# Kernel tuning notes

Measured on AMD Instinct MI355X. Metric: run time of the kernel, lower is better.

The kernel has to match this reference:

```python
import jax, jax.numpy as jnp
import numpy as np
from jax import lax

B, P, ENC = 64, 196, 2048
E, H, A, V = 512, 512, 512, 10000
L = 21  # caption length -> T = 20 decode steps


def setup_inputs() -> dict:
    key = jax.random.key(0)
    ks = jax.random.split(key, 20)
    s = 0.02
    inp = {
        "features": jax.random.normal(ks[0], (B, P, ENC), jnp.float32),
        "captions": jax.random.randint(ks[1], (B, L), 0, V),
        # attention
        "W_enc_att": jax.random.normal(ks[2], (ENC, A), jnp.float32) * s,
        "b_enc_att": jnp.zeros((A,), jnp.float32),
        "W_dec_att": jax.random.normal(ks[3], (H, A), jnp.float32) * s,
        "b_dec_att": jnp.zeros((A,), jnp.float32),
        "W_full": jax.random.normal(ks[4], (A, 1), jnp.float32) * s,
        "b_full": jnp.zeros((1,), jnp.float32),
        # embedding (uniform(-0.1, 0.1) as in init_weights)
        "emb": jax.random.uniform(ks[5], (V, E), jnp.float32, -0.1, 0.1),
        # LSTMCell: input = embed + encoder_dim, gate order i,f,g,o
        "W_ih": jax.random.normal(ks[6], (E + ENC, 4 * H), jnp.float32) * s,
        "W_hh": jax.random.normal(ks[7], (H, 4 * H), jnp.float32) * s,
        "b_ih": jnp.zeros((4 * H,), jnp.float32),
        "b_hh": jnp.zeros((4 * H,), jnp.float32),
        # init state projections
        "W_init_h": jax.random.normal(ks[8], (ENC, H), jnp.float32) * s,
        "b_init_h": jnp.zeros((H,), jnp.float32),
        "W_init_c": jax.random.normal(ks[9], (ENC, H), jnp.float32) * s,
        "b_init_c": jnp.zeros((H,), jnp.float32),
        # gating
        "W_fbeta": jax.random.normal(ks[10], (H, ENC), jnp.float32) * s,
        "b_fbeta": jnp.zeros((ENC,), jnp.float32),
        # output fc (uniform(-0.1,0.1), bias 0)
        "W_fc": jax.random.uniform(ks[11], (H, V), jnp.float32, -0.1, 0.1),
        "b_fc": jnp.zeros((V,), jnp.float32),
    }
    return inp


def reference(features, captions, W_enc_att, b_enc_att, W_dec_att, b_dec_att,
              W_full, b_full, emb, W_ih, W_hh, b_ih, b_hh,
              W_init_h, b_init_h, W_init_c, b_init_c,
              W_fbeta, b_fbeta, W_fc, b_fc):
    # init hidden state from mean-pooled encoder features
    mean_enc = features.mean(axis=1)                       # [B, ENC]
    h0 = mean_enc @ W_init_h + b_init_h                    # [B, H]
    c0 = mean_enc @ W_init_c + b_init_c

    # encoder-side attention projection is time-invariant: precompute
    att1 = features @ W_enc_att + b_enc_att                # [B, P, A]

    T = captions.shape[1] - 1                              # decode_lengths = L-1 (equal lengths)
    embs = emb[captions[:, :T]]                            # [B, T, E]
    embs_t = jnp.swapaxes(embs, 0, 1)                      # [T, B, E]

    def step(carry, e_t):
        h, c = carry
        att2 = h @ W_dec_att + b_dec_att                   # [B, A]
        scores = (jax.nn.relu(att1 + att2[:, None, :]) @ W_full)[..., 0] + b_full  # [B, P]
        alpha = jax.nn.softmax(scores, axis=1)
        awe = jnp.einsum('bp,bpe->be', alpha, features)    # [B, ENC]
        gate = jax.nn.sigmoid(h @ W_fbeta + b_fbeta)
        awe = gate * awe
        x = jnp.concatenate([e_t, awe], axis=1)            # [B, E+ENC]
        gates = x @ W_ih + h @ W_hh + b_ih + b_hh          # [B, 4H]
        i, f, g, o = jnp.split(gates, 4, axis=1)
        c_new = jax.nn.sigmoid(f) * c + jax.nn.sigmoid(i) * jnp.tanh(g)
        h_new = jax.nn.sigmoid(o) * jnp.tanh(c_new)
        preds = h_new @ W_fc + b_fc                        # dropout in eval mode = identity
        return (h_new, c_new), preds

    _, preds = lax.scan(step, (h0, c0), embs_t)            # [T, B, V]
    return jnp.swapaxes(preds, 0, 1)                       # [B, T, V]
```

## Files before the change

### kernel.cpp

```cpp
#include <hip/hip_runtime.h>
#include <hip/hip_bf16.h>


#define TB 256

typedef __bf16 bf16x8 __attribute__((ext_vector_type(8)));
typedef float f32x4 __attribute__((ext_vector_type(4)));
typedef unsigned short u16x8 __attribute__((ext_vector_type(8)));
typedef unsigned short u16x4 __attribute__((ext_vector_type(4)));
typedef unsigned short ushort_t;

__device__ __forceinline__ ushort_t f2bf(float x) {
    unsigned u = __builtin_bit_cast(unsigned, x);
    u += 0x7fffu + ((u >> 16) & 1u);
    return (ushort_t)(u >> 16);
}
__device__ __forceinline__ float bf2f(ushort_t b) {
    return __builtin_bit_cast(float, (unsigned)b << 16);
}
__device__ __forceinline__ void store_pack(
    ushort_t* __restrict__ Ph, ushort_t* __restrict__ Pl,
    int KC, int m, int k, float v)
{
    const size_t flat = ((((size_t)(m >> 4) * KC + (k >> 5)) * 64)
                         + ((k & 31) >> 3) * 16 + (m & 15)) * 8 + (k & 7);
    const ushort_t h = f2bf(v);
    Ph[flat] = h;
    Pl[flat] = f2bf(v - bf2f(h));
}

struct PackJobs {
    const float* W[7];
    ushort_t* Bh[7];
    ushort_t* Bl[7];
    int Nsrc[7], ntCount[7], KC[7], ntBase[7];
    int cum[8];
};

__global__ __launch_bounds__(TB) void pack_all(PackJobs J)
{
    const int blk = blockIdx.x;
    int j = 0;
    #pragma unroll
    for (int i = 1; i < 7; ++i) if (blk >= J.cum[i]) j = i;
    const int g = (blk - J.cum[j]) * TB + threadIdx.x;
    const int KC = J.KC[j];
    const int lane = g & 63;
    const int kc = (g >> 6) % KC;
    const int nt = g / (64 * KC);
    if (nt >= J.ntCount[j]) return;
    const int Nsrc = J.Nsrc[j];
    const float* W = J.W[j];
    const int n = nt * 16 + (lane & 15);
    const int kb = kc * 32 + (lane >> 4) * 8;
    u16x8 hv, lv;
    #pragma unroll
    for (int e = 0; e < 8; ++e) {
        const float x = (n < Nsrc) ? W[(size_t)(kb + e) * Nsrc + n] : 0.f;
        const ushort_t h = f2bf(x);
        hv[e] = h;
        lv[e] = f2bf(x - bf2f(h));
    }
    const size_t flat = (((size_t)(J.ntBase[j] + nt) * KC + kc) * 64 + lane) * 8;
    *(u16x8*)&J.Bh[j][flat] = hv;
    *(u16x8*)&J.Bl[j][flat] = lv;
}

__global__ __launch_bounds__(TB) void feat2bf(
    const float* __restrict__ f, ushort_t* __restrict__ fbf)
{
    const size_t i8 = ((size_t)blockIdx.x * TB + threadIdx.x) * 8;
    const float4 a = *(const float4*)&f[i8];
    const float4 b = *(const float4*)&f[i8 + 4];
    u16x8 v;
    v[0] = f2bf(a.x); v[1] = f2bf(a.y); v[2] = f2bf(a.z); v[3] = f2bf(a.w);
    v[4] = f2bf(b.x); v[5] = f2bf(b.y); v[6] = f2bf(b.z); v[7] = f2bf(b.w);
    *(u16x8*)&fbf[i8] = v;
}

template<int MT, int NT, int WR, int WC>
__device__ __forceinline__ void mfma_tile(
    const ushort_t* lds, int wr, int wc, int lane,
    f32x4 acc[MT / WR][NT / WC])
{
    constexpr int MFR = MT / WR, NFR = NT / WC;
    bf16x8 ah[MFR], al[MFR];
    #pragma unroll
    for (int i = 0; i < MFR; ++i) {
        ah[i] = __builtin_bit_cast(bf16x8, *(const u16x8*)&lds[(wr * MFR + i) * 512 + lane * 8]);
        al[i] = __builtin_bit_cast(bf16x8, *(const u16x8*)&lds[(MT + wr * MFR + i) * 512 + lane * 8]);
    }
    #pragma unroll
    for (int j = 0; j < NFR; ++j) {
        const bf16x8 bh = __builtin_bit_cast(bf16x8, *(const u16x8*)&lds[(2 * MT + wc * NFR + j) * 512 + lane * 8]);
        const bf16x8 bl = __builtin_bit_cast(bf16x8, *(const u16x8*)&lds[(2 * MT + NT + wc * NFR + j) * 512 + lane * 8]);
        #pragma unroll
        for (int i = 0; i < MFR; ++i) {
            acc[i][j] = __builtin_amdgcn_mfma_f32_16x16x32_bf16(ah[i], bh, acc[i][j], 0, 0, 0);
            acc[i][j] = __builtin_amdgcn_mfma_f32_16x16x32_bf16(ah[i], bl, acc[i][j], 0, 0, 0);
            acc[i][j] = __builtin_amdgcn_mfma_f32_16x16x32_bf16(al[i], bh, acc[i][j], 0, 0, 0);
        }
    }
}

template<int MT, int NT, int WR, int WC>
__global__ __launch_bounds__(TB) void gemm_mfma(
    const ushort_t* __restrict__ Ah, const ushort_t* __restrict__ Al,
    const ushort_t* __restrict__ Bh, const ushort_t* __restrict__ Bl,
    int KC, int kcPer,
    const float* __restrict__ bias,
    float* __restrict__ C, int ldc, int Ncols, size_t cPartStride)
{
    constexpr int MFR = MT / WR, NFR = NT / WC, CH = 2 * (MT + NT);
    __shared__ __align__(16) ushort_t lds[CH * 512];
    const int tid = threadIdx.x, wid = tid >> 6, lane = tid & 63;
    const int wr = wid / WC, wc = wid % WC;

    const int tot = gridDim.x * gridDim.y;
    const int lin = blockIdx.x + gridDim.x * blockIdx.y;
    const int q = tot >> 3, r = tot & 7;
    const int xcd = lin & 7, jj = lin >> 3;
    const int base = (xcd < r) ? xcd * (q + 1) : r * (q + 1) + (xcd - r) * q;
    const int lin2 = base + jj;
    const int nb = lin2 / gridDim.y;
    const int mb = lin2 % gridDim.y;

    const int kc0 = blockIdx.z * kcPer;

    f32x4 acc[MFR][NFR];
    #pragma unroll
    for (int i = 0; i < MFR; ++i)
        #pragma unroll
        for (int j = 0; j < NFR; ++j)
            acc[i][j] = f32x4{0.f, 0.f, 0.f, 0.f};

    for (int kc = kc0; kc < kc0 + kcPer; ++kc) {
        __syncthreads();
        #pragma unroll
        for (int cc = 0; cc < CH / 4; ++cc) {
            const int c = cc * 4 + wid;
            const ushort_t* src;
            if (c < MT)                src = Ah + ((size_t)(mb * MT + c) * KC + kc) * 512;
            else if (c < 2 * MT)       src = Al + ((size_t)(mb * MT + c - MT) * KC + kc) * 512;
            else if (c < 2 * MT + NT)  src = Bh + ((size_t)(nb * NT + c - 2 * MT) * KC + kc) * 512;
            else                       src = Bl + ((size_t)(nb * NT + c - 2 * MT - NT) * KC + kc) * 512;
            *(u16x8*)&lds[c * 512 + lane * 8] = *(const u16x8*)(src + lane * 8);
        }
        __syncthreads();
        mfma_tile<MT, NT, WR, WC>(lds, wr, wc, lane, acc);
    }

    C += (size_t)blockIdx.z * cPartStride;
    #pragma unroll
    for (int i = 0; i < MFR; ++i)
        #pragma unroll
        for (int j = 0; j < NFR; ++j) {
            const int col = nb * NT * 16 + (wc * NFR + j) * 16 + (lane & 15);
            if (col < Ncols) {
                const float bv = bias ? bias[col] : 0.f;
                const int rbase = mb * MT * 16 + (wr * MFR + i) * 16 + ((lane >> 4) << 2);
                #pragma unroll
                for (int r2 = 0; r2 < 4; ++r2)
                    C[(size_t)(rbase + r2) * ldc + col] = acc[i][j][r2] + bv;
            }
        }
}

__global__ __launch_bounds__(TB) void gemm_att1(
    const ushort_t* __restrict__ fbf,
    const ushort_t* __restrict__ Bh, const ushort_t* __restrict__ Bl,
    const float* __restrict__ bias, ushort_t* __restrict__ att1bf)
{
    __shared__ __align__(16) ushort_t lds[20 * 512];
    const int tid = threadIdx.x, wid = tid >> 6, lane = tid & 63;
    const int wr = wid >> 1, wc = wid & 1;

    const int lin = blockIdx.x + (blockIdx.y << 2);
    const int lin2 = (lin & 7) * 98 + (lin >> 3);
    const int nb = lin2 & 3, mb = lin2 >> 2;

    f32x4 acc[2][4];
    #pragma unroll
    for (int i = 0; i < 2; ++i)
        #pragma unroll
        for (int j = 0; j < 4; ++j)
            acc[i][j] = f32x4{0.f, 0.f, 0.f, 0.f};

    const int arow = tid >> 2, akg = tid & 3;
    const size_t abase = (size_t)(mb * 64 + arow) * 2048 + akg * 8;
    const int aldst = (arow >> 4) * 512 + (akg * 16 + (arow & 15)) * 8;

    for (int kc = 0; kc < 64; ++kc) {
        __syncthreads();
        #pragma unroll
        for (int cc = 0; cc < 4; ++cc) {
            const int c = cc * 4 + wid;
            const ushort_t* src = (c < 8)
                ? Bh + ((size_t)(nb * 8 + c) * 64 + kc) * 512
                : Bl + ((size_t)(nb * 8 + c - 8) * 64 + kc) * 512;
            *(u16x8*)&lds[(4 + c) * 512 + lane * 8] = *(const u16x8*)(src + lane * 8);
        }
        *(u16x8*)&lds[aldst] = *(const u16x8*)&fbf[abase + (size_t)kc * 32];
        __syncthreads();

        bf16x8 ah[2];
        #pragma unroll
        for (int i = 0; i < 2; ++i)
            ah[i] = __builtin_bit_cast(bf16x8, *(const u16x8*)&lds[(wr * 2 + i) * 512 + lane * 8]);
        #pragma unroll
        for (int j = 0; j < 4; ++j) {
            const bf16x8 bh = __builtin_bit_cast(bf16x8, *(const u16x8*)&lds[(4 + wc * 4 + j) * 512 + lane * 8]);
            const bf16x8 bl = __builtin_bit_cast(bf16x8, *(const u16x8*)&lds[(12 + wc * 4 + j) * 512 + lane * 8]);
            #pragma unroll
            for (int i = 0; i < 2; ++i) {
                acc[i][j] = __builtin_amdgcn_mfma_f32_16x16x32_bf16(ah[i], bh, acc[i][j], 0, 0, 0);
                acc[i][j] = __builtin_amdgcn_mfma_f32_16x16x32_bf16(ah[i], bl, acc[i][j], 0, 0, 0);
            }
        }
    }

    #pragma unroll
    for (int i = 0; i < 2; ++i)
        #pragma unroll
        for (int j = 0; j < 4; ++j) {
            const int col = nb * 128 + (wc * 4 + j) * 16 + (lane & 15);
            const float bv = bias[col];
            const int rbase = mb * 64 + (wr * 2 + i) * 16 + ((lane >> 4) << 2);
            #pragma unroll
            for (int r = 0; r < 4; ++r)
                att1bf[(size_t)(rbase + r) * 512 + col] = f2bf(acc[i][j][r] + bv);
        }
}

__device__ __forceinline__ void gemm_body(
    float (*As)[68], float (*Ws)[68],
    const float* __restrict__ A, int lda,
    const float* __restrict__ W, int ldw,
    float* __restrict__ C, int ldc,
    int nTile, int N, int K)
{
    const int tid = threadIdx.x;
    const int tn = tid & 15;
    const int tm = tid >> 4;
    const int n0 = nTile * 64;

    float acc[4][4] = {{0.f}};

    for (int k0 = 0; k0 < K; k0 += 32) {
        {
            int r  = tid >> 3;
            int cc = (tid & 7) * 4;
            #pragma unroll
            for (int rr = 0; rr < 64; rr += 32) {
                const float4 a = *(const float4*)&A[(size_t)(rr + r) * lda + (k0 + cc)];
                As[cc + 0][rr + r] = a.x;
                As[cc + 1][rr + r] = a.y;
                As[cc + 2][rr + r] = a.z;
                As[cc + 3][rr + r] = a.w;
            }
        }
        {
            int r  = tid >> 4;
            int cc = (tid & 15) * 4;
            #pragma unroll
            for (int rr = 0; rr < 32; rr += 16) {
                const float4 w = *(const float4*)&W[(size_t)(k0 + rr + r) * ldw + (n0 + cc)];
                *(float4*)&Ws[rr + r][cc] = w;
            }
        }
        __syncthreads();
        #pragma unroll
        for (int kk = 0; kk < 32; ++kk) {
            const float4 a = *(const float4*)&As[kk][tm * 4];
            const float4 w = *(const float4*)&Ws[kk][tn * 4];
            const float av[4] = {a.x, a.y, a.z, a.w};
            const float wv[4] = {w.x, w.y, w.z, w.w};
            #pragma unroll
            for (int i = 0; i < 4; ++i)
                #pragma unroll
                for (int j = 0; j < 4; ++j)
                    acc[i][j] = fmaf(av[i], wv[j], acc[i][j]);
        }
        __syncthreads();
    }

    #pragma unroll
    for (int i = 0; i < 4; ++i) {
        const int m = tm * 4 + i;
        #pragma unroll
        for (int j = 0; j < 4; ++j)
            C[(size_t)m * ldc + (n0 + tn * 4 + j)] = acc[i][j];
    }
}

__global__ __launch_bounds__(TB) void gemm_hc(
    const float* __restrict__ mean,
    const float* __restrict__ Wh0, const float* __restrict__ Wc0,
    float* __restrict__ h0p, float* __restrict__ c0p)
{
    __shared__ float As[32][68];
    __shared__ float Ws[32][68];
    const int ks = blockIdx.y & 7;
    const int which = blockIdx.y >> 3;
    const float* W = which ? Wc0 : Wh0;
    float* Cp = which ? c0p : h0p;
    gemm_body(As, Ws,
              mean + (size_t)ks * 256, 2048,
              W + (size_t)ks * 256 * 512, 512,
              Cp + (size_t)ks * 64 * 512, 512,
              blockIdx.x, 512, 256);
}

__global__ __launch_bounds__(TB) void scores_k(
    const ushort_t* __restrict__ att1bf,
    const float* __restrict__ hga_part,
    const float* __restrict__ bd,
    const float* __restrict__ Wfull,
    float* __restrict__ scores)
{
    const int b = blockIdx.x;
    const int tid = threadIdx.x;
    const int wave = tid >> 6;
    const int lane = tid & 63;

    __shared__ float a2[512];
    __shared__ float wf[512];

    for (int i = tid; i < 512; i += TB) {
        float v = bd[i];
        #pragma unroll
        for (int s = 0; s < 4; ++s)
            v += hga_part[(size_t)s * 64 * 4608 + (size_t)b * 4608 + i];
        a2[i] = v;
        wf[i] = Wfull[i];
    }
    __syncthreads();

    const int k0 = lane * 8;
    float a2r[8], wfr[8];
    #pragma unroll
    for (int e = 0; e < 8; ++e) { a2r[e] = a2[k0 + e]; wfr[e] = wf[k0 + e]; }

    const int p0 = blockIdx.y * 28 + wave * 7;
    #pragma unroll
    for (int pp = 0; pp < 7; ++pp) {
        const int p = p0 + pp;
        const u16x8 v = *(const u16x8*)&att1bf[((size_t)b * 196 + p) * 512 + k0];
        float s = 0.f;
        #pragma unroll
        for (int e = 0; e < 8; ++e)
            s = fmaf(fmaxf(bf2f(v[e]) + a2r[e], 0.f), wfr[e], s);
        #pragma unroll
        for (int o = 32; o; o >>= 1) s += __shfl_xor(s, o);
        if (lane == 0) scores[b * 196 + p] = s;
    }
}

__global__ __launch_bounds__(512) void awe_gate(
    const float* __restrict__ scores,
    const ushort_t* __restrict__ fbf,
    const float* __restrict__ hga_part,
    const float* __restrict__ bf,
    ushort_t* __restrict__ gPh, ushort_t* __restrict__ gPl)
{
    const int b = blockIdx.y, chunk = blockIdx.x;
    const int tid = threadIdx.x;
    const int q = tid >> 6, lane = tid & 63;

    __shared__ float al[196];
    __shared__ float redm[8], reds[8];
    __shared__ float smq[8][512];

    const float sv = (tid < 196) ? scores[b * 196 + tid] : -1e30f;
    float m = sv;
    #pragma unroll
    for (int o = 32; o; o >>= 1) m = fmaxf(m, __shfl_xor(m, o));
    if (lane == 0) redm[q] = m;
    __syncthreads();
    m = redm[0];
    #pragma unroll
    for (int i = 1; i < 8; ++i) m = fmaxf(m, redm[i]);

    const float e = (tid < 196) ? expf(sv - m) : 0.f;
    float s = e;
    #pragma unroll
    for (int o = 32; o; o >>= 1) s += __shfl_xor(s, o);
    if (lane == 0) reds[q] = s;
    __syncthreads();
    s = reds[0];
    #pragma unroll
    for (int i = 1; i < 8; ++i) s += reds[i];

    if (tid < 196) al[tid] = e / s;
    __syncthreads();

    const int col0 = chunk * 512 + lane * 8;
    const ushort_t* f = fbf + (size_t)b * 196 * 2048 + col0;
    float acc[8] = {0.f, 0.f, 0.f, 0.f, 0.f, 0.f, 0.f, 0.f};
    const int p0 = q * 25;
    const int pn = (q == 7) ? 21 : 25;
    for (int pp = 0; pp < pn; ++pp) {
        const float w = al[p0 + pp];
        const u16x8 v = *(const u16x8*)&f[(size_t)(p0 + pp) * 2048];
        #pragma unroll
        for (int ee = 0; ee < 8; ++ee)
            acc[ee] = fmaf(w, bf2f(v[ee]), acc[ee]);
    }
    *(f32x4*)&smq[q][lane * 8]     = f32x4{acc[0], acc[1], acc[2], acc[3]};
    *(f32x4*)&smq[q][lane * 8 + 4] = f32x4{acc[4], acc[5], acc[6], acc[7]};
    __syncthreads();

    const int eg = chunk * 512 + tid;
    float a = smq[0][tid];
    #pragma unroll
    for (int i = 1; i < 8; ++i) a += smq[i][tid];
    float gp = bf[eg];
    #pragma unroll
    for (int ss = 0; ss < 4; ++ss)
        gp += hga_part[(size_t)ss * 64 * 4608 + (size_t)b * 4608 + 512 + eg];
    const float gate = 1.f / (1.f + expf(-gp));
    store_pack(gPh, gPl, 64, b, eg, gate * a);
}

__global__ __launch_bounds__(TB) void lstm_pw(
    const float* __restrict__ gates_part,
    const float* __restrict__ hga_part,
    const float* __restrict__ eW,
    const float* __restrict__ b_hh,
    int t,
    float* __restrict__ c,
    ushort_t* __restrict__ hPh, ushort_t* __restrict__ hPl,
    ushort_t* __restrict__ sPh, ushort_t* __restrict__ sPl)
{
    const int idx = blockIdx.x * TB + threadIdx.x;
    const int b = idx >> 9;
    const int j = idx & 511;

    float g[4];
    #pragma unroll
    for (int comp = 0; comp < 4; ++comp) {
        const int col = comp * 512 + j;
        float v = b_hh[col] + eW[((size_t)b * 20 + t) * 2048 + col];
        #pragma unroll
        for (int s = 0; s < 8; ++s)
            v += gates_part[(size_t)s * 64 * 2048 + (size_t)b * 2048 + col];
        #pragma unroll
        for (int s = 0; s < 4; ++s)
            v += hga_part[(size_t)s * 64 * 4608 + (size_t)b * 4608 + 2560 + col];
        g[comp] = v;
    }
    const float si = 1.f / (1.f + expf(-g[0]));
    const float sf = 1.f / (1.f + expf(-g[1]));
    const float gg = tanhf(g[2]);
    const float so = 1.f / (1.f + expf(-g[3]));
    const float cn = sf * c[idx] + si * gg;
    c[idx] = cn;
    const float hn = so * tanhf(cn);
    store_pack(hPh, hPl, 16, b, j, hn);
    store_pack(sPh, sPl, 16, b * 20 + t, j, hn);
}

__global__ __launch_bounds__(TB) void mean_feat(
    const float* __restrict__ features, float* __restrict__ mean_enc)
{
    const int b = blockIdx.y;
    const int e = blockIdx.x * TB + threadIdx.x;
    const float* f = features + (size_t)b * 196 * 2048 + e;
    float s = 0.f;
    #pragma unroll 4
    for (int p = 0; p < 196; ++p) s += f[(size_t)p * 2048];
    mean_enc[b * 2048 + e] = s * (1.f / 196.f);
}

__global__ __launch_bounds__(TB) void gather_emb_pack(
    const int* __restrict__ captions,
    const float* __restrict__ emb,
    ushort_t* __restrict__ Ph, ushort_t* __restrict__ Pl)
{
    const int bt = blockIdx.x;
    const int b = bt / 20;
    const int t = bt % 20;
    const int tok = captions[b * 21 + t];
    for (int e = threadIdx.x; e < 512; e += TB)
        store_pack(Ph, Pl, 16, bt, e, emb[(size_t)tok * 512 + e]);
}

__global__ __launch_bounds__(TB) void reduce_hc(
    const float* __restrict__ h0p, const float* __restrict__ c0p,
    const float* __restrict__ bh0, const float* __restrict__ bc0,
    ushort_t* __restrict__ hPh, ushort_t* __restrict__ hPl,
    float* __restrict__ c)
{
    const int idx = blockIdx.x * TB + threadIdx.x;
    const int half = idx >> 15;
    const int i = idx & 32767;
    const int j = i & 511;
    const float* P = half ? c0p : h0p;
    float v = half ? bc0[j] : bh0[j];
    #pragma unroll
    for (int s = 0; s < 8; ++s) v += P[(size_t)s * 64 * 512 + i];
    if (half) c[i] = v;
    else      store_pack(hPh, hPl, 16, i >> 9, j, v);
}

extern "C" void kernel_launch(void* const* d_in, const int* in_sizes, int n_in,
                              void* d_out, int out_size, void* d_ws, size_t ws_size,
                              hipStream_t stream)
{
    const float* features  = (const float*)d_in[0];
    const int*   captions  = (const int*)  d_in[1];
    const float* W_enc_att = (const float*)d_in[2];
    const float* b_enc_att = (const float*)d_in[3];
    const float* W_dec_att = (const float*)d_in[4];
    const float* b_dec_att = (const float*)d_in[5];
    const float* W_full    = (const float*)d_in[6];
    const float* emb       = (const float*)d_in[8];
    const float* W_ih      = (const float*)d_in[9];
    const float* W_hh      = (const float*)d_in[10];
    const float* b_ih      = (const float*)d_in[11];
    const float* b_hh      = (const float*)d_in[12];
    const float* W_init_h  = (const float*)d_in[13];
    const float* b_init_h  = (const float*)d_in[14];
    const float* W_init_c  = (const float*)d_in[15];
    const float* b_init_c  = (const float*)d_in[16];
    const float* W_fbeta   = (const float*)d_in[17];
    const float* b_fbeta   = (const float*)d_in[18];
    const float* W_fc      = (const float*)d_in[19];
    const float* b_fc      = (const float*)d_in[20];
    float* out = (float*)d_out;
    (void)ws_size;

    float* ws = (float*)d_ws;
    size_t off = 0;
    auto alloc  = [&](size_t n) { float* p = ws + off; off += n; return p; };
    auto ualloc = [&](size_t n) { ushort_t* p = (ushort_t*)(ws + off); off += (n + 1) / 2; return p; };

    float* eW     = alloc((size_t)64 * 20 * 2048);
    float* mean   = alloc(64 * 2048);
    float* hga    = alloc((size_t)4 * 64 * 4608);
    float* gatesp = alloc((size_t)8 * 64 * 2048);
    float* c      = alloc(64 * 512);
    float* scores = alloc(64 * 196);

    ushort_t* fbf    = ualloc((size_t)12544 * 2048);
    ushort_t* att1bf = ualloc((size_t)12544 * 512);
    ushort_t* WencH = ualloc((size_t)32 * 64 * 512);
    ushort_t* WencL = ualloc((size_t)32 * 64 * 512);
    ushort_t* WtopH = ualloc((size_t)128 * 16 * 512);
    ushort_t* WtopL = ualloc((size_t)128 * 16 * 512);
    ushort_t* Wih2H = ualloc((size_t)128 * 64 * 512);
    ushort_t* Wih2L = ualloc((size_t)128 * 64 * 512);
    ushort_t* WdfhH = ualloc((size_t)288 * 16 * 512);
    ushort_t* WdfhL = ualloc((size_t)288 * 16 * 512);
    ushort_t* WfcH  = ualloc((size_t)632 * 16 * 512);
    ushort_t* WfcL  = ualloc((size_t)632 * 16 * 512);
    ushort_t* embsH = ualloc((size_t)80 * 16 * 512);
    ushort_t* embsL = ualloc((size_t)80 * 16 * 512);
    ushort_t* hPh   = ualloc((size_t)4 * 16 * 512);
    ushort_t* hPl   = ualloc((size_t)4 * 16 * 512);
    ushort_t* gPh   = ualloc((size_t)4 * 64 * 512);
    ushort_t* gPl   = ualloc((size_t)4 * 64 * 512);
    ushort_t* sPh   = ualloc((size_t)80 * 16 * 512);
    ushort_t* sPl   = ualloc((size_t)80 * 16 * 512);

    float* h0p = hga;
    float* c0p = gatesp;

    PackJobs J;
    J.W[0]=W_enc_att;               J.Bh[0]=WencH; J.Bl[0]=WencL; J.Nsrc[0]=512;   J.ntCount[0]=32;  J.KC[0]=64; J.ntBase[0]=0;
    J.W[1]=W_ih;                    J.Bh[1]=WtopH; J.Bl[1]=WtopL; J.Nsrc[1]=2048;  J.ntCount[1]=128; J.KC[1]=16; J.ntBase[1]=0;
    J.W[2]=W_ih + (size_t)512*2048; J.Bh[2]=Wih2H; J.Bl[2]=Wih2L; J.Nsrc[2]=2048;  J.ntCount[2]=128; J.KC[2]=64; J.ntBase[2]=0;
    J.W[3]=W_dec_att;               J.Bh[3]=WdfhH; J.Bl[3]=WdfhL; J.Nsrc[3]=512;   J.ntCount[3]=32;  J.KC[3]=16; J.ntBase[3]=0;
    J.W[4]=W_fbeta;                 J.Bh[4]=WdfhH; J.Bl[4]=WdfhL; J.Nsrc[4]=2048;  J.ntCount[4]=128; J.KC[4]=16; J.ntBase[4]=32;
    J.W[5]=W_hh;                    J.Bh[5]=WdfhH; J.Bl[5]=WdfhL; J.Nsrc[5]=2048;  J.ntCount[5]=128; J.KC[5]=16; J.ntBase[5]=160;
    J.W[6]=W_fc;                    J.Bh[6]=WfcH;  J.Bl[6]=WfcL;  J.Nsrc[6]=10000; J.ntCount[6]=632; J.KC[6]=16; J.ntBase[6]=0;
    {
        int cum = 0;
        const int blks[7] = {512, 512, 2048, 128, 512, 512, 2528};
        for (int i = 0; i < 7; ++i) { J.cum[i] = cum; cum += blks[i]; }
        J.cum[7] = cum;
        pack_all<<<cum, TB, 0, stream>>>(J);
    }

    feat2bf<<<12544, TB, 0, stream>>>(features, fbf);
    gather_emb_pack<<<1280, TB, 0, stream>>>(captions, emb, embsH, embsL);
    mean_feat<<<dim3(8, 64), TB, 0, stream>>>(features, mean);
    gemm_hc<<<dim3(8, 16), TB, 0, stream>>>(mean, W_init_h, W_init_c, h0p, c0p);
    reduce_hc<<<256, TB, 0, stream>>>(h0p, c0p, b_init_h, b_init_c, hPh, hPl, c);
    gemm_att1<<<dim3(4, 196), TB, 0, stream>>>(fbf, WencH, WencL, b_enc_att, att1bf);
    gemm_mfma<8, 8, 2, 2><<<dim3(16, 10, 1), TB, 0, stream>>>(
        embsH, embsL, WtopH, WtopL, 16, 16, b_ih, eW, 2048, 2048, 0);

    for (int t = 0; t < 20; ++t) {
        gemm_mfma<4, 8, 2, 2><<<dim3(36, 1, 4), TB, 0, stream>>>(
            hPh, hPl, WdfhH, WdfhL, 16, 4, nullptr, hga, 4608, 4608, (size_t)64 * 4608);
        scores_k<<<dim3(64, 7), TB, 0, stream>>>(att1bf, hga, b_dec_att, W_full, scores);
        awe_gate<<<dim3(4, 64), 512, 0, stream>>>(scores, fbf, hga, b_fbeta, gPh, gPl);
        gemm_mfma<4, 8, 2, 2><<<dim3(16, 1, 8), TB, 0, stream>>>(
            gPh, gPl, Wih2H, Wih2L, 64, 8, nullptr, gatesp, 2048, 2048, (size_t)64 * 2048);
        lstm_pw<<<128, TB, 0, stream>>>(gatesp, hga, eW, b_hh, t, c, hPh, hPl, sPh, sPl);
    }

    gemm_mfma<8, 8, 2, 2><<<dim3(79, 10, 1), TB, 0, stream>>>(
        sPh, sPl, WfcH, WfcL, 16, 16, b_fc, out, 10000, 10000, 0);
}
```

Before: 1.056 ms.

## Double-buffer att1 GEMM LDS with register prefetch; compute mean from bf16 features

gemm_att1 now processes two K-chunks per iteration into a double-buffered LDS region. It prefetches the next tiles into registers while the MFMAs run on the current buffer, which halves the barriers and hides global load latency. mean_feat now reads the bf16 copy of the features instead of fp32, halving the bytes it reads. The bf16 mean adds rounding error to the initial h/c, and the larger LDS footprint may reduce occupancy.

Measured after the change: 1.051 ms. About the same (-0.4%).

```diff
diff --git a/kernel.cpp b/kernel.cpp
--- a/kernel.cpp
+++ b/kernel.cpp
@@ -171,7 +171,7 @@
     const ushort_t* __restrict__ Bh, const ushort_t* __restrict__ Bl,
     const float* __restrict__ bias, ushort_t* __restrict__ att1bf)
 {
-    __shared__ __align__(16) ushort_t lds[20 * 512];
+    __shared__ __align__(16) ushort_t lds[2 * 40 * 512];
     const int tid = threadIdx.x, wid = tid >> 6, lane = tid & 63;
     const int wr = wid >> 1, wc = wid & 1;
 
@@ -188,35 +188,65 @@
 
     const int arow = tid >> 2, akg = tid & 3;
     const size_t abase = (size_t)(mb * 64 + arow) * 2048 + akg * 8;
-    const int aldst = (arow >> 4) * 512 + (akg * 16 + (arow & 15)) * 8;
-
-    for (int kc = 0; kc < 64; ++kc) {
+    const int aldst = (akg * 16 + (arow & 15)) * 8;
+    const int achunk = arow >> 4;
+
+    u16x8 regs[10];
+
+    auto issue = [&](int kc2) {
+        #pragma unroll
+        for (int cc = 0; cc < 8; ++cc) {
+            const int s = cc * 4 + wid;
+            const int kcoff = s & 1, ch = s >> 1;
+            const ushort_t* src = (ch < 8)
+                ? Bh + ((size_t)(nb * 8 + ch) * 64 + kc2 + kcoff) * 512
+                : Bl + ((size_t)(nb * 8 + (ch - 8)) * 64 + kc2 + kcoff) * 512;
+            regs[cc] = *(const u16x8*)(src + lane * 8);
+        }
+        regs[8] = *(const u16x8*)&fbf[abase + (size_t)kc2 * 32];
+        regs[9] = *(const u16x8*)&fbf[abase + (size_t)(kc2 + 1) * 32];
+    };
+    auto commit = [&](ushort_t* buf) {
+        #pragma unroll
+        for (int cc = 0; cc < 8; ++cc) {
+            const int s = cc * 4 + wid;
+            *(u16x8*)&buf[(8 + s) * 512 + lane * 8] = regs[cc];
+        }
+        *(u16x8*)&buf[achunk * 512 + aldst] = regs[8];
+        *(u16x8*)&buf[(4 + achunk) * 512 + aldst] = regs[9];
+    };
+
+    issue(0);
+    commit(lds);
+    __syncthreads();
+
+    int cur = 0;
+    for (int kc2 = 0; kc2 < 64; kc2 += 2) {
+        const bool more = (kc2 + 2 < 64);
+        if (more) issue(kc2 + 2);
+
+        const ushort_t* buf = lds + cur * 40 * 512;
+        #pragma unroll
+        for (int kcoff = 0; kcoff < 2; ++kcoff) {
+            bf16x8 ah[2];
+            #pragma unroll
+            for (int i = 0; i < 2; ++i)
+                ah[i] = __builtin_bit_cast(bf16x8, *(const u16x8*)&buf[(kcoff * 4 + wr * 2 + i) * 512 + lane * 8]);
+            #pragma unroll
+            for (int j = 0; j < 4; ++j) {
+                const bf16x8 bh = __builtin_bit_cast(bf16x8, *(const u16x8*)&buf[(8 + (wc * 4 + j) * 2 + kcoff) * 512 + lane * 8]);
+                const bf16x8 bl = __builtin_bit_cast(bf16x8, *(const u16x8*)&buf[(8 + (8 + wc * 4 + j) * 2 + kcoff) * 512 + lane * 8]);
+                #pragma unroll
+                for (int i = 0; i < 2; ++i) {
+                    acc[i][j] = __builtin_amdgcn_mfma_f32_16x16x32_bf16(ah[i], bh, acc[i][j], 0, 0, 0);
+                    acc[i][j] = __builtin_amdgcn_mfma_f32_16x16x32_bf16(ah[i], bl, acc[i][j], 0, 0, 0);
+                }
+            }
+        }
+
+        if (more) commit(lds + (cur ^ 1) * 40 * 512);
         __syncthreads();
-        #pragma unroll
-        for (int cc = 0; cc < 4; ++cc) {
-            const int c = cc * 4 + wid;
-            const ushort_t* src = (c < 8)
-                ? Bh + ((size_t)(nb * 8 + c) * 64 + kc) * 512
-                : Bl + ((size_t)(nb * 8 + c - 8) * 64 + kc) * 512;
-            *(u16x8*)&lds[(4 + c) * 512 + lane * 8] = *(const u16x8*)(src + lane * 8);
-        }
-        *(u16x8*)&lds[aldst] = *(const u16x8*)&fbf[abase + (size_t)kc * 32];
-        __syncthreads();
-
-        bf16x8 ah[2];
-        #pragma unroll
-        for (int i = 0; i < 2; ++i)
-            ah[i] = __builtin_bit_cast(bf16x8, *(const u16x8*)&lds[(wr * 2 + i) * 512 + lane * 8]);
-        #pragma unroll
-        for (int j = 0; j < 4; ++j) {
-            const bf16x8 bh = __builtin_bit_cast(bf16x8, *(const u16x8*)&lds[(4 + wc * 4 + j) * 512 + lane * 8]);
-            const bf16x8 bl = __builtin_bit_cast(bf16x8, *(const u16x8*)&lds[(12 + wc * 4 + j) * 512 + lane * 8]);
-            #pragma unroll
-            for (int i = 0; i < 2; ++i) {
-                acc[i][j] = __builtin_amdgcn_mfma_f32_16x16x32_bf16(ah[i], bh, acc[i][j], 0, 0, 0);
-                acc[i][j] = __builtin_amdgcn_mfma_f32_16x16x32_bf16(ah[i], bl, acc[i][j], 0, 0, 0);
-            }
-        }
+        cur ^= 1;
     }
 
     #pragma unroll
@@ -460,15 +490,15 @@
     store_pack(sPh, sPl, 16, b * 20 + t, j, hn);
 }
 
-__global__ __launch_bounds__(TB) void mean_feat(
-    const float* __restrict__ features, float* __restrict__ mean_enc)
+__global__ __launch_bounds__(TB) void mean_feat_bf(
+    const ushort_t* __restrict__ fbf, float* __restrict__ mean_enc)
 {
     const int b = blockIdx.y;
     const int e = blockIdx.x * TB + threadIdx.x;
-    const float* f = features + (size_t)b * 196 * 2048 + e;
+    const ushort_t* f = fbf + (size_t)b * 196 * 2048 + e;
     float s = 0.f;
     #pragma unroll 4
-    for (int p = 0; p < 196; ++p) s += f[(size_t)p * 2048];
+    for (int p = 0; p < 196; ++p) s += bf2f(f[(size_t)p * 2048]);
     mean_enc[b * 2048 + e] = s * (1.f / 196.f);
 }
 
@@ -584,7 +614,7 @@
 
     feat2bf<<<12544, TB, 0, stream>>>(features, fbf);
     gather_emb_pack<<<1280, TB, 0, stream>>>(captions, emb, embsH, embsL);
-    mean_feat<<<dim3(8, 64), TB, 0, stream>>>(features, mean);
+    mean_feat_bf<<<dim3(8, 64), TB, 0, stream>>>(fbf, mean);
     gemm_hc<<<dim3(8, 16), TB, 0, stream>>>(mean, W_init_h, W_init_c, h0p, c0p);
     reduce_hc<<<256, TB, 0, stream>>>(h0p, c0p, b_init_h, b_init_c, hPh, hPl, c);
     gemm_att1<<<dim3(4, 196), TB, 0, stream>>>(fbf, WencH, WencL, b_enc_att, att1bf);
```

## Double-buffer att1 GEMM with register prefetch, larger M tile, bf16 mean

Applied to the files above, without the earlier changes.

Rewrites the encoder attention projection GEMM to use a 128-row M tile. It double-buffers LDS with a register prefetch of the next K chunk, so global loads overlap MFMA work and half as many blocks are launched. The grid swizzle and launch dims are adjusted to match. Separately, the mean-pooling kernel now reads the bf16 copy of features instead of fp32, halving its memory traffic at a small precision cost. The GEMM change uses more registers and LDS, which may reduce occupancy.

Result: no change. 1.036 ms (-1.9%).

```diff
diff --git a/kernel.cpp b/kernel.cpp
--- a/kernel.cpp
+++ b/kernel.cpp
@@ -171,61 +171,93 @@
     const ushort_t* __restrict__ Bh, const ushort_t* __restrict__ Bl,
     const float* __restrict__ bias, ushort_t* __restrict__ att1bf)
 {
-    __shared__ __align__(16) ushort_t lds[20 * 512];
+    __shared__ __align__(16) ushort_t lds[2 * 24 * 512];
     const int tid = threadIdx.x, wid = tid >> 6, lane = tid & 63;
     const int wr = wid >> 1, wc = wid & 1;
 
     const int lin = blockIdx.x + (blockIdx.y << 2);
-    const int lin2 = (lin & 7) * 98 + (lin >> 3);
+    const int lin2 = (lin & 7) * 49 + (lin >> 3);
     const int nb = lin2 & 3, mb = lin2 >> 2;
 
-    f32x4 acc[2][4];
-    #pragma unroll
-    for (int i = 0; i < 2; ++i)
+    f32x4 acc[4][4];
+    #pragma unroll
+    for (int i = 0; i < 4; ++i)
         #pragma unroll
         for (int j = 0; j < 4; ++j)
             acc[i][j] = f32x4{0.f, 0.f, 0.f, 0.f};
 
     const int arow = tid >> 2, akg = tid & 3;
-    const size_t abase = (size_t)(mb * 64 + arow) * 2048 + akg * 8;
-    const int aldst = (arow >> 4) * 512 + (akg * 16 + (arow & 15)) * 8;
-
-    for (int kc = 0; kc < 64; ++kc) {
-        __syncthreads();
+    const size_t abase = (size_t)(mb * 128) * 2048;
+
+    u16x8 rA[6], rB[6];
+
+    auto issueTo = [&](int kc, u16x8* r) {
         #pragma unroll
         for (int cc = 0; cc < 4; ++cc) {
             const int c = cc * 4 + wid;
             const ushort_t* src = (c < 8)
                 ? Bh + ((size_t)(nb * 8 + c) * 64 + kc) * 512
-                : Bl + ((size_t)(nb * 8 + c - 8) * 64 + kc) * 512;
-            *(u16x8*)&lds[(4 + c) * 512 + lane * 8] = *(const u16x8*)(src + lane * 8);
-        }
-        *(u16x8*)&lds[aldst] = *(const u16x8*)&fbf[abase + (size_t)kc * 32];
-        __syncthreads();
-
-        bf16x8 ah[2];
-        #pragma unroll
-        for (int i = 0; i < 2; ++i)
-            ah[i] = __builtin_bit_cast(bf16x8, *(const u16x8*)&lds[(wr * 2 + i) * 512 + lane * 8]);
+                : Bl + ((size_t)(nb * 8 + (c - 8)) * 64 + kc) * 512;
+            r[cc] = *(const u16x8*)(src + lane * 8);
+        }
+        #pragma unroll
+        for (int p = 0; p < 2; ++p) {
+            const int row = (p * 256 + tid) >> 2;
+            r[4 + p] = *(const u16x8*)&fbf[abase + (size_t)row * 2048 + (size_t)kc * 32 + akg * 8];
+        }
+    };
+    auto commitFrom = [&](const u16x8* r, ushort_t* buf) {
+        #pragma unroll
+        for (int cc = 0; cc < 4; ++cc) {
+            const int c = cc * 4 + wid;
+            *(u16x8*)&buf[(8 + c) * 512 + lane * 8] = r[cc];
+        }
+        #pragma unroll
+        for (int p = 0; p < 2; ++p) {
+            const int row = (p * 256 + tid) >> 2;
+            *(u16x8*)&buf[(row >> 4) * 512 + (akg * 16 + (row & 15)) * 8] = r[4 + p];
+        }
+    };
+    auto compute = [&](const ushort_t* buf) {
+        bf16x8 ah[4];
+        #pragma unroll
+        for (int i = 0; i < 4; ++i)
+            ah[i] = __builtin_bit_cast(bf16x8, *(const u16x8*)&buf[(wr * 4 + i) * 512 + lane * 8]);
         #pragma unroll
         for (int j = 0; j < 4; ++j) {
-            const bf16x8 bh = __builtin_bit_cast(bf16x8, *(const u16x8*)&lds[(4 + wc * 4 + j) * 512 + lane * 8]);
-            const bf16x8 bl = __builtin_bit_cast(bf16x8, *(const u16x8*)&lds[(12 + wc * 4 + j) * 512 + lane * 8]);
+            const bf16x8 bh = __builtin_bit_cast(bf16x8, *(const u16x8*)&buf[(8 + wc * 4 + j) * 512 + lane * 8]);
+            const bf16x8 bl = __builtin_bit_cast(bf16x8, *(const u16x8*)&buf[(16 + wc * 4 + j) * 512 + lane * 8]);
             #pragma unroll
-            for (int i = 0; i < 2; ++i) {
+            for (int i = 0; i < 4; ++i) {
                 acc[i][j] = __builtin_amdgcn_mfma_f32_16x16x32_bf16(ah[i], bh, acc[i][j], 0, 0, 0);
                 acc[i][j] = __builtin_amdgcn_mfma_f32_16x16x32_bf16(ah[i], bl, acc[i][j], 0, 0, 0);
             }
         }
-    }
-
-    #pragma unroll
-    for (int i = 0; i < 2; ++i)
+    };
+
+    issueTo(0, rA);
+    commitFrom(rA, lds);
+    issueTo(1, rB);
+    __syncthreads();
+
+    for (int kc = 0; kc < 64; kc += 2) {
+        if (kc + 2 < 64) issueTo(kc + 2, rA);
+        compute(lds);
+        commitFrom(rB, lds + 24 * 512);
+        __syncthreads();
+        if (kc + 3 < 64) issueTo(kc + 3, rB);
+        compute(lds + 24 * 512);
+        if (kc + 2 < 64) commitFrom(rA, lds);
+        __syncthreads();
+    }
+
+    #pragma unroll
+    for (int i = 0; i < 4; ++i)
         #pragma unroll
         for (int j = 0; j < 4; ++j) {
             const int col = nb * 128 + (wc * 4 + j) * 16 + (lane & 15);
             const float bv = bias[col];
-            const int rbase = mb * 64 + (wr * 2 + i) * 16 + ((lane >> 4) << 2);
+            const int rbase = mb * 128 + (wr * 4 + i) * 16 + ((lane >> 4) << 2);
             #pragma unroll
             for (int r = 0; r < 4; ++r)
                 att1bf[(size_t)(rbase + r) * 512 + col] = f2bf(acc[i][j][r] + bv);
@@ -460,15 +492,15 @@
     store_pack(sPh, sPl, 16, b * 20 + t, j, hn);
 }
 
-__global__ __launch_bounds__(TB) void mean_feat(
-    const float* __restrict__ features, float* __restrict__ mean_enc)
+__global__ __launch_bounds__(TB) void mean_feat_bf(
+    const ushort_t* __restrict__ fbf, float* __restrict__ mean_enc)
 {
     const int b = blockIdx.y;
     const int e = blockIdx.x * TB + threadIdx.x;
-    const float* f = features + (size_t)b * 196 * 2048 + e;
+    const ushort_t* f = fbf + (size_t)b * 196 * 2048 + e;
     float s = 0.f;
     #pragma unroll 4
-    for (int p = 0; p < 196; ++p) s += f[(size_t)p * 2048];
+    for (int p = 0; p < 196; ++p) s += bf2f(f[(size_t)p * 2048]);
     mean_enc[b * 2048 + e] = s * (1.f / 196.f);
 }
 
@@ -584,10 +616,10 @@
 
     feat2bf<<<12544, TB, 0, stream>>>(features, fbf);
     gather_emb_pack<<<1280, TB, 0, stream>>>(captions, emb, embsH, embsL);
-    mean_feat<<<dim3(8, 64), TB, 0, stream>>>(features, mean);
+    mean_feat_bf<<<dim3(8, 64), TB, 0, stream>>>(fbf, mean);
     gemm_hc<<<dim3(8, 16), TB, 0, stream>>>(mean, W_init_h, W_init_c, h0p, c0p);
     reduce_hc<<<256, TB, 0, stream>>>(h0p, c0p, b_init_h, b_init_c, hPh, hPl, c);
-    gemm_att1<<<dim3(4, 196), TB, 0, stream>>>(fbf, WencH, WencL, b_enc_att, att1bf);
+    gemm_att1<<<dim3(4, 98), TB, 0, stream>>>(fbf, WencH, WencL, b_enc_att, att1bf);
     gemm_mfma<8, 8, 2, 2><<<dim3(16, 10, 1), TB, 0, stream>>>(
         embsH, embsL, WtopH, WtopL, 16, 16, b_ih, eW, 2048, 2048, 0);
 
```
